# Optimization experiments

Hardware: AMD Instinct MI355X
Metric: run time of the kernel (lower is better)

Reference implementation:

```python
import jax, jax.numpy as jnp
import numpy as np

PS = 4          # patch size
C = 3           # channels
VOCAB = 512
D = 256         # embed dim
PD = PS * PS * C  # 48 patch dim


def _gelu(x):
    return jax.nn.gelu(x, approximate=False)  # torch nn.GELU default = exact erf


def setup_inputs() -> dict:
    key = jax.random.key(0)
    ks = jax.random.split(key, 16)
    frames = jax.random.uniform(ks[0], (32, 256, 256, 3), jnp.float32) * 255.0

    def lin(kw, kb, fan_in, fan_out):
        bound = 1.0 / np.sqrt(fan_in)
        w = jax.random.uniform(kw, (fan_out, fan_in), jnp.float32, -bound, bound)
        b = jax.random.uniform(kb, (fan_out,), jnp.float32, -bound, bound)
        return w, b

    enc_w1, enc_b1 = lin(ks[1], ks[2], PD, D)
    enc_w2, enc_b2 = lin(ks[3], ks[4], D, D)
    enc_w3, enc_b3 = lin(ks[5], ks[6], D, D)
    dec_w1, dec_b1 = lin(ks[7], ks[8], D, D)
    dec_w2, dec_b2 = lin(ks[9], ks[10], D, D)
    dec_w3, dec_b3 = lin(ks[11], ks[12], D, PD)
    codebook = jax.random.normal(ks[13], (VOCAB, D), jnp.float32) * 0.1
    return {
        'frames': frames,
        'enc_w1': enc_w1, 'enc_b1': enc_b1,
        'enc_w2': enc_w2, 'enc_b2': enc_b2,
        'enc_w3': enc_w3, 'enc_b3': enc_b3,
        'codebook': codebook,
        'dec_w1': dec_w1, 'dec_b1': dec_b1,
        'dec_w2': dec_w2, 'dec_b2': dec_b2,
        'dec_w3': dec_w3, 'dec_b3': dec_b3,
    }


def _patchify(x):  # [B,H,W,C] -> [B, N, ps*ps*C]
    B, H, W, Ch = x.shape
    h, w = H // PS, W // PS
    x = x.reshape(B, h, PS, w, PS, Ch).transpose(0, 1, 3, 2, 4, 5)
    return x.reshape(B, h * w, PS * PS * Ch)


def _unpatchify(p):  # [B, N, ps*ps*C] -> [B,H,W,C]
    B, N, _ = p.shape
    h = w = int(np.sqrt(N))
    p = p.reshape(B, h, w, PS, PS, C).transpose(0, 1, 3, 2, 4, 5)
    return p.reshape(B, h * PS, w * PS, C)


def reference(frames, enc_w1, enc_b1, enc_w2, enc_b2, enc_w3, enc_b3,
              codebook, dec_w1, dec_b1, dec_w2, dec_b2, dec_w3, dec_b3):
    x = frames / 255.0 * 2.0 - 1.0
    patches = _patchify(x)  # [B,N,48]
    # encoder MLP
    z = _gelu(patches @ enc_w1.T + enc_b1)
    z = _gelu(z @ enc_w2.T + enc_b2)
    z_e = z @ enc_w3.T + enc_b3  # [B,N,D]
    # nearest-codebook lookup (squared L2; argmin equals cdist argmin)
    d2 = (jnp.sum(z_e * z_e, -1, keepdims=True)
          - 2.0 * jnp.einsum('bnd,vd->bnv', z_e, codebook)
          + jnp.sum(codebook * codebook, -1))  # [B,N,V]
    tokens = jnp.argmin(d2, axis=-1)  # [B,N] int
    z_q = codebook[tokens]  # [B,N,D]
    z_q_st = z_e + jax.lax.stop_gradient(z_q - z_e)
    # decoder MLP
    y = _gelu(z_q_st @ dec_w1.T + dec_b1)
    y = _gelu(y @ dec_w2.T + dec_b2)
    y = y @ dec_w3.T + dec_b3  # [B,N,48]
    recon = _unpatchify(y)
    target = frames / 255.0 * 2.0 - 1.0
    recon_loss = jnp.mean((recon - target) ** 2)
    commitment_loss = jnp.mean((z_e - jax.lax.stop_gradient(z_q)) ** 2)
    codebook_loss = jnp.mean((z_q - jax.lax.stop_gradient(z_e)) ** 2)
    return recon, tokens, recon_loss, commitment_loss, codebook_loss
```

## Files before the change

### kernel.cpp

```cpp
#include <hip/hip_runtime.h>
#include <hip/hip_bf16.h>
#include <math.h>
#include <float.h>
#include <limits.h>

#define T_ROWS 131072

typedef __attribute__((ext_vector_type(8))) short short8;
typedef __attribute__((ext_vector_type(4))) float f32x4;

__device__ __forceinline__ float gelu_f(float x){
    return 0.5f * x * (1.0f + erff(x * 0.7071067811865475f));
}
__device__ __forceinline__ float bf2f(ushort u){
    union { unsigned int i; float f; } v; v.i = ((unsigned int)u) << 16; return v.f;
}
__device__ __forceinline__ ushort f2bf(float f){
    union { float f; unsigned int i; } v; v.f = f;
    unsigned int i = v.i;
    unsigned int r = (i + 0x7fffu + ((i >> 16) & 1u)) >> 16;
    return (ushort)r;
}
__device__ __forceinline__ void split3(float x, ushort &u0, ushort &u1, ushort &u2){
    union { float f; unsigned int i; } v; v.f = x;
    u0 = (ushort)(v.i >> 16);
    union { unsigned int i; float f; } h0; h0.i = ((unsigned int)u0) << 16;
    float r = x - h0.f;
    union { float f; unsigned int i; } vr; vr.f = r;
    u1 = (ushort)(vr.i >> 16);
    union { unsigned int i; float f; } h1; h1.i = ((unsigned int)u1) << 16;
    float r2 = r - h1.f;
    union { float f; unsigned int i; } v2; v2.f = r2;
    u2 = (ushort)(v2.i >> 16);
}

__global__ __launch_bounds__(256) void prep_kernel(
    const float* __restrict__ w2, const float* __restrict__ w3,
    const float* __restrict__ d1, const float* __restrict__ d2,
    const float* __restrict__ w1, const float* __restrict__ b1,
    const float* __restrict__ cb,
    ushort* __restrict__ w2s0, ushort* __restrict__ w2s1, ushort* __restrict__ w2s2,
    ushort* __restrict__ w3s0, ushort* __restrict__ w3s1, ushort* __restrict__ w3s2,
    ushort* __restrict__ w1b, ushort* __restrict__ w2b,
    float* __restrict__ cn, ushort* __restrict__ cbb,
    ushort* __restrict__ cbs0, ushort* __restrict__ cbs1, ushort* __restrict__ cbs2,
    ushort* __restrict__ w1p0, ushort* __restrict__ w1p1, ushort* __restrict__ w1p2,
    float* __restrict__ bias2)
{
    const int blk = blockIdx.x, tid = threadIdx.x;
    if (blk < 64){
        const int i = (blk*256 + tid)*4;
        float4 a = *(const float4*)(w2 + i);
        ushort4 s0, s1, s2;
        split3(a.x, s0.x, s1.x, s2.x); split3(a.y, s0.y, s1.y, s2.y);
        split3(a.z, s0.z, s1.z, s2.z); split3(a.w, s0.w, s1.w, s2.w);
        *(ushort4*)(w2s0+i)=s0; *(ushort4*)(w2s1+i)=s1; *(ushort4*)(w2s2+i)=s2;
        float4 b = *(const float4*)(w3 + i);
        split3(b.x, s0.x, s1.x, s2.x); split3(b.y, s0.y, s1.y, s2.y);
        split3(b.z, s0.z, s1.z, s2.z); split3(b.w, s0.w, s1.w, s2.w);
        *(ushort4*)(w3s0+i)=s0; *(ushort4*)(w3s1+i)=s1; *(ushort4*)(w3s2+i)=s2;
        float4 c = *(const float4*)(d1 + i);
        ushort4 u; u.x=f2bf(c.x); u.y=f2bf(c.y); u.z=f2bf(c.z); u.w=f2bf(c.w);
        *(ushort4*)(w1b+i) = u;
        float4 d = *(const float4*)(d2 + i);
        u.x=f2bf(d.x); u.y=f2bf(d.y); u.z=f2bf(d.z); u.w=f2bf(d.w);
        *(ushort4*)(w2b+i) = u;
    } else if (blk < 192){
        const int lane = tid & 63;
        const int code = (blk-64)*4 + (tid >> 6);
        float4 v = ((const float4*)(cb + (size_t)code*256))[lane];
        size_t off = (size_t)code*256 + lane*4;
        ushort4 u; u.x=f2bf(v.x); u.y=f2bf(v.y); u.z=f2bf(v.z); u.w=f2bf(v.w);
        *(ushort4*)(cbb + off) = u;
        ushort4 s0, s1, s2;
        split3(v.x, s0.x, s1.x, s2.x); split3(v.y, s0.y, s1.y, s2.y);
        split3(v.z, s0.z, s1.z, s2.z); split3(v.w, s0.w, s1.w, s2.w);
        *(ushort4*)(cbs0 + off) = s0;
        *(ushort4*)(cbs1 + off) = s1;
        *(ushort4*)(cbs2 + off) = s2;
        float s = v.x*v.x + v.y*v.y + v.z*v.z + v.w*v.w;
        #pragma unroll
        for (int m=1; m<64; m<<=1) s += __shfl_xor(s, m);
        if (lane == 0) cn[code] = s;
    } else if (blk < 208){
        const int idx = (blk-192)*256 + tid;
        const int n = idx >> 4, k = (idx & 15)*4;
        ushort4 s0 = {0,0,0,0}, s1 = {0,0,0,0}, s2 = {0,0,0,0};
        if (k < 48){
            float4 v = *(const float4*)(w1 + n*48 + k);
            split3(v.x, s0.x, s1.x, s2.x); split3(v.y, s0.y, s1.y, s2.y);
            split3(v.z, s0.z, s1.z, s2.z); split3(v.w, s0.w, s1.w, s2.w);
        }
        *(ushort4*)(w1p0 + n*64 + k) = s0;
        *(ushort4*)(w1p1 + n*64 + k) = s1;
        *(ushort4*)(w1p2 + n*64 + k) = s2;
    } else {
        float s = 0.0f;
        for (int k=0;k<48;++k) s += w1[tid*48 + k];
        bias2[tid] = b1[tid] - s;
    }
}

template<int KTOT, bool GELU, int LOADER, bool SCALE>
__global__ __launch_bounds__(256, 3) void split6_gemm(
    const float* __restrict__ Ain,
    const float* __restrict__ frames,
    const ushort* __restrict__ W0, const ushort* __restrict__ W1,
    const ushort* __restrict__ W2,
    const float* __restrict__ bias,
    float* __restrict__ Cout)
{
    __shared__ __align__(16) ushort Al[3][64][40];
    __shared__ __align__(16) ushort Wl[256][40];

    const int tid = threadIdx.x;
    const int m0 = blockIdx.x * 64;
    const int arow = tid >> 2, q = tid & 3;
    const int lane = tid & 63;
    const int w = tid >> 6;
    const int lr = lane & 15, lg = lane >> 4;

    const float* asrc = nullptr;
    int pbase = 0;
    if constexpr (LOADER == 0){
        asrc = Ain + (size_t)(m0 + arow)*KTOT + q*8;
    } else {
        int p = m0 + arow;
        int b = p >> 12, nl = p & 4095, hh = nl >> 6, ww = nl & 63;
        pbase = ((b*256 + hh*4)*256 + ww*4)*3;
    }
    const ushort* wsrc  = W0 + (size_t)tid*KTOT;
    const ushort* w1frag = W1 + (size_t)(w*64 + lr)*KTOT + lg*8;
    const ushort* w2frag = W2 + (size_t)(w*64 + lr)*KTOT + lg*8;

    f32x4 acc[4][4];
    #pragma unroll
    for (int mi=0;mi<4;++mi)
        #pragma unroll
        for (int ni=0;ni<4;++ni)
            acc[mi][ni] = (f32x4){0.f,0.f,0.f,0.f};

    for (int k0=0; k0<KTOT; k0+=32){
        float x[8];
        if constexpr (LOADER == 0){
            *(float4*)&x[0] = *(const float4*)(asrc + k0);
            *(float4*)&x[4] = *(const float4*)(asrc + k0 + 4);
        } else {
            #pragma unroll
            for (int j=0;j<2;++j){
                int kk = k0 + q*8 + j*4;
                float4 v = {0.f,0.f,0.f,0.f};
                if (kk < 48){
                    int ph = kk/12, rem = kk - ph*12;
                    v = *(const float4*)(frames + pbase + ph*768 + rem);
                }
                x[j*4+0]=v.x; x[j*4+1]=v.y; x[j*4+2]=v.z; x[j*4+3]=v.w;
            }
        }
        ushort t0[8], t1[8], t2[8];
        #pragma unroll
        for (int e=0;e<8;++e) split3(x[e], t0[e], t1[e], t2[e]);
        *(uint4*)&Al[0][arow][q*8] = *(const uint4*)t0;
        *(uint4*)&Al[1][arow][q*8] = *(const uint4*)t1;
        *(uint4*)&Al[2][arow][q*8] = *(const uint4*)t2;
        *(uint4*)&Wl[tid][0]  = *(const uint4*)(wsrc + k0);
        *(uint4*)&Wl[tid][8]  = *(const uint4*)(wsrc + k0 + 8);
        *(uint4*)&Wl[tid][16] = *(const uint4*)(wsrc + k0 + 16);
        *(uint4*)&Wl[tid][24] = *(const uint4*)(wsrc + k0 + 24);
        short8 b1v[4], b2v[4];
        #pragma unroll
        for (int ni=0;ni<4;++ni){
            b1v[ni] = *(const short8*)(w1frag + (size_t)ni*16*KTOT + k0);
            b2v[ni] = *(const short8*)(w2frag + (size_t)ni*16*KTOT + k0);
        }
        __syncthreads();

        short8 b0v[4];
        #pragma unroll
        for (int ni=0;ni<4;++ni)
            b0v[ni] = *(const short8*)&Wl[w*64 + ni*16 + lr][lg*8];
        #pragma unroll
        for (int mi=0;mi<4;++mi){
            short8 a0 = *(const short8*)&Al[0][mi*16 + lr][lg*8];
            short8 a1 = *(const short8*)&Al[1][mi*16 + lr][lg*8];
            short8 a2 = *(const short8*)&Al[2][mi*16 + lr][lg*8];
            #pragma unroll
            for (int ni=0;ni<4;++ni)
                acc[mi][ni] = __builtin_amdgcn_mfma_f32_16x16x32_bf16(a0, b0v[ni], acc[mi][ni], 0,0,0);
            #pragma unroll
            for (int ni=0;ni<4;++ni)
                acc[mi][ni] = __builtin_amdgcn_mfma_f32_16x16x32_bf16(a0, b1v[ni], acc[mi][ni], 0,0,0);
            #pragma unroll
            for (int ni=0;ni<4;++ni)
                acc[mi][ni] = __builtin_amdgcn_mfma_f32_16x16x32_bf16(a1, b0v[ni], acc[mi][ni], 0,0,0);
            #pragma unroll
            for (int ni=0;ni<4;++ni)
                acc[mi][ni] = __builtin_amdgcn_mfma_f32_16x16x32_bf16(a0, b2v[ni], acc[mi][ni], 0,0,0);
            #pragma unroll
            for (int ni=0;ni<4;++ni)
                acc[mi][ni] = __builtin_amdgcn_mfma_f32_16x16x32_bf16(a1, b1v[ni], acc[mi][ni], 0,0,0);
            #pragma unroll
            for (int ni=0;ni<4;++ni)
                acc[mi][ni] = __builtin_amdgcn_mfma_f32_16x16x32_bf16(a2, b0v[ni], acc[mi][ni], 0,0,0);
        }
        __syncthreads();
    }

    const float alpha = 2.0f/255.0f;
    float bn[4];
    #pragma unroll
    for (int ni=0;ni<4;++ni) bn[ni] = bias[w*64 + ni*16 + lr];
    #pragma unroll
    for (int mi=0;mi<4;++mi)
        #pragma unroll
        for (int ni=0;ni<4;++ni)
            #pragma unroll
            for (int r=0;r<4;++r){
                int row = m0 + mi*16 + lg*4 + r;
                float v;
                if (SCALE) v = fmaf(alpha, acc[mi][ni][r], bn[ni]);
                else       v = acc[mi][ni][r] + bn[ni];
                if (GELU) v = gelu_f(v);
                Cout[(size_t)row*256 + w*64 + ni*16 + lr] = v;
            }
}

#define INSERT1(dv, iv) do { \
    float _d = (dv); int _i = (iv); \
    if (_d < bd || (_d == bd && _i < bi)){ bd = _d; bi = _i; } \
} while(0)

__global__ __launch_bounds__(256, 3) void tokens_split6(
    const float* __restrict__ Zf,
    const ushort* __restrict__ C0, const ushort* __restrict__ C1,
    const ushort* __restrict__ C2,
    const float* __restrict__ cn,
    float2* __restrict__ partials,
    float* __restrict__ zz_out)
{
    __shared__ __align__(16) ushort Al[3][128][40];
    __shared__ __align__(16) ushort Wl[2][128][40];
    __shared__ float2 ptop[128][2];

    const int tid = threadIdx.x;
    const int m0 = blockIdx.x * 128;
    const int n0 = blockIdx.y * 128;
    const int srow = tid >> 1, shalf = (tid & 1) * 16;
    const int lane = tid & 63;
    const int w = tid >> 6;
    const int wm = (w >> 1) * 64, wn = (w & 1) * 64;
    const int lr = lane & 15, lg = lane >> 4;

    const float*  asrc = Zf + (size_t)(m0 + srow)*256 + shalf;
    const ushort* ws0  = C0 + (size_t)(n0 + srow)*256 + shalf;
    const ushort* ws1  = C1 + (size_t)(n0 + srow)*256 + shalf;
    const ushort* c2frag = C2 + (size_t)(n0 + wn + lr)*256 + lg*8;

    f32x4 acc[4][4];
    #pragma unroll
    for (int mi=0;mi<4;++mi)
        #pragma unroll
        for (int ni=0;ni<4;++ni)
            acc[mi][ni] = (f32x4){0.f,0.f,0.f,0.f};

    float zzp = 0.0f;

    for (int k0=0; k0<256; k0+=32){
        float x[16];
        *(float4*)&x[0]  = *(const float4*)(asrc + k0);
        *(float4*)&x[4]  = *(const float4*)(asrc + k0 + 4);
        *(float4*)&x[8]  = *(const float4*)(asrc + k0 + 8);
        *(float4*)&x[12] = *(const float4*)(asrc + k0 + 12);
        ushort t0[16], t1[16], t2[16];
        #pragma unroll
        for (int e=0;e<16;++e){
            split3(x[e], t0[e], t1[e], t2[e]);
            zzp = fmaf(x[e], x[e], zzp);
        }
        *(uint4*)&Al[0][srow][shalf]   = *(const uint4*)&t0[0];
        *(uint4*)&Al[0][srow][shalf+8] = *(const uint4*)&t0[8];
        *(uint4*)&Al[1][srow][shalf]   = *(const uint4*)&t1[0];
        *(uint4*)&Al[1][srow][shalf+8] = *(const uint4*)&t1[8];
        *(uint4*)&Al[2][srow][shalf]   = *(const uint4*)&t2[0];
        *(uint4*)&Al[2][srow][shalf+8] = *(const uint4*)&t2[8];
        *(uint4*)&Wl[0][srow][shalf]   = *(const uint4*)(ws0 + k0);
        *(uint4*)&Wl[0][srow][shalf+8] = *(const uint4*)(ws0 + k0 + 8);
        *(uint4*)&Wl[1][srow][shalf]   = *(const uint4*)(ws1 + k0);
        *(uint4*)&Wl[1][srow][shalf+8] = *(const uint4*)(ws1 + k0 + 8);
        short8 b2[4];
        #pragma unroll
        for (int ni=0;ni<4;++ni)
            b2[ni] = *(const short8*)(c2frag + (size_t)ni*16*256 + k0);
        __syncthreads();

        short8 b0[4], b1[4];
        #pragma unroll
        for (int ni=0;ni<4;++ni){
            b0[ni] = *(const short8*)&Wl[0][wn + ni*16 + lr][lg*8];
            b1[ni] = *(const short8*)&Wl[1][wn + ni*16 + lr][lg*8];
        }
        #pragma unroll
        for (int mi=0;mi<4;++mi){
            short8 a0 = *(const short8*)&Al[0][wm + mi*16 + lr][lg*8];
            short8 a1 = *(const short8*)&Al[1][wm + mi*16 + lr][lg*8];
            short8 a2 = *(const short8*)&Al[2][wm + mi*16 + lr][lg*8];
            #pragma unroll
            for (int ni=0;ni<4;++ni)
                acc[mi][ni] = __builtin_amdgcn_mfma_f32_16x16x32_bf16(a0, b0[ni], acc[mi][ni], 0,0,0);
            #pragma unroll
            for (int ni=0;ni<4;++ni)
                acc[mi][ni] = __builtin_amdgcn_mfma_f32_16x16x32_bf16(a0, b1[ni], acc[mi][ni], 0,0,0);
            #pragma unroll
            for (int ni=0;ni<4;++ni)
                acc[mi][ni] = __builtin_amdgcn_mfma_f32_16x16x32_bf16(a1, b0[ni], acc[mi][ni], 0,0,0);
            #pragma unroll
            for (int ni=0;ni<4;++ni)
                acc[mi][ni] = __builtin_amdgcn_mfma_f32_16x16x32_bf16(a0, b2[ni], acc[mi][ni], 0,0,0);
            #pragma unroll
            for (int ni=0;ni<4;++ni)
                acc[mi][ni] = __builtin_amdgcn_mfma_f32_16x16x32_bf16(a1, b1[ni], acc[mi][ni], 0,0,0);
            #pragma unroll
            for (int ni=0;ni<4;++ni)
                acc[mi][ni] = __builtin_amdgcn_mfma_f32_16x16x32_bf16(a2, b0[ni], acc[mi][ni], 0,0,0);
        }
        __syncthreads();
    }

    {
        float other = __shfl_xor(zzp, 1);
        if (blockIdx.y == 0 && (tid & 1) == 0)
            zz_out[m0 + srow] = zzp + other;
    }

    float cnl[4];
    #pragma unroll
    for (int ni=0;ni<4;++ni) cnl[ni] = cn[n0 + wn + ni*16 + lr];

    #pragma unroll
    for (int mi=0;mi<4;++mi)
        #pragma unroll
        for (int r=0;r<4;++r){
            float bd = FLT_MAX; int bi = INT_MAX;
            #pragma unroll
            for (int ni=0;ni<4;++ni){
                float d = cnl[ni] - 2.0f*acc[mi][ni][r];
                int col = n0 + wn + ni*16 + lr;
                INSERT1(d, col);
            }
            #pragma unroll
            for (int m=1; m<16; m<<=1){
                float od = __shfl_xor(bd, m);
                int   oi = __shfl_xor(bi, m);
                INSERT1(od, oi);
            }
            if (lr == 0)
                ptop[wm + mi*16 + lg*4 + r][w & 1] = make_float2(bd, (float)bi);
        }
    __syncthreads();
    if (tid < 128){
        float2 hA = ptop[tid][0], hB = ptop[tid][1];
        int   gA = (int)hA.y, gB = (int)hB.y;
        bool takeB = (hB.x < hA.x) || (hB.x == hA.x && gB < gA);
        partials[(size_t)(m0 + tid)*4 + blockIdx.y] = takeB ? hB : hA;
    }
}

__global__ __launch_bounds__(256) void token_reduce(
    const float* __restrict__ zz_out, const float2* __restrict__ partials,
    float* __restrict__ tokf, float* __restrict__ loss)
{
    const int tid = threadIdx.x;
    const int row = blockIdx.x*256 + tid;
    float2 p0 = partials[(size_t)row*4 + 0];
    float2 p1 = partials[(size_t)row*4 + 1];
    float2 p2 = partials[(size_t)row*4 + 2];
    float2 p3 = partials[(size_t)row*4 + 3];
    float d = p0.x; int g = (int)p0.y;
    if (p1.x < d || (p1.x == d && (int)p1.y < g)){ d = p1.x; g = (int)p1.y; }
    if (p2.x < d || (p2.x == d && (int)p2.y < g)){ d = p2.x; g = (int)p2.y; }
    if (p3.x < d || (p3.x == d && (int)p3.y < g)){ d = p3.x; g = (int)p3.y; }
    tokf[row] = (float)g;
    float cs = zz_out[row] + d;
    #pragma unroll
    for (int m=1; m<64; m<<=1) cs += __shfl_xor(cs, m);
    __shared__ float wsum[4];
    const int lane = tid & 63, w = tid >> 6;
    if (lane == 0) wsum[w] = cs;
    __syncthreads();
    if (tid == 0) atomicAdd(loss + 1, wsum[0]+wsum[1]+wsum[2]+wsum[3]);
}

template<int LOADER>
__global__ __launch_bounds__(256) void mfma_gemm(
    const ushort* __restrict__ Abf,
    const ushort* __restrict__ cbb,
    const float* __restrict__ tokf,
    const ushort* __restrict__ Wbf,
    const float* __restrict__ bias,
    ushort* __restrict__ Ybf)
{
    __shared__ __align__(16) ushort Al[128][40];
    __shared__ __align__(16) ushort Wl[128][40];

    const int tid = threadIdx.x;
    const int m0 = blockIdx.x * 128;
    const int n0 = blockIdx.y * 128;
    const int srow = tid >> 1, shalf = (tid & 1) * 16;
    const int lane = tid & 63;
    const int w = tid >> 6;
    const int wm = (w >> 1) * 64, wn = (w & 1) * 64;
    const int lr = lane & 15, lg = lane >> 4;

    const ushort* asrc;
    if constexpr (LOADER == 1){
        int g = (int)tokf[m0 + srow];
        asrc = cbb + (size_t)g*256 + shalf;
    } else {
        asrc = Abf + (size_t)(m0 + srow)*256 + shalf;
    }
    const ushort* wsrc = Wbf + (size_t)(n0 + srow)*256 + shalf;

    f32x4 acc[4][4];
    #pragma unroll
    for (int mi=0;mi<4;++mi)
        #pragma unroll
        for (int ni=0;ni<4;++ni)
            acc[mi][ni] = (f32x4){0.f,0.f,0.f,0.f};

    for (int k0=0; k0<256; k0+=32){
        *(uint4*)&Al[srow][shalf]   = *(const uint4*)(asrc + k0);
        *(uint4*)&Al[srow][shalf+8] = *(const uint4*)(asrc + k0 + 8);
        *(uint4*)&Wl[srow][shalf]   = *(const uint4*)(wsrc + k0);
        *(uint4*)&Wl[srow][shalf+8] = *(const uint4*)(wsrc + k0 + 8);
        __syncthreads();

        short8 af[4], bfr[4];
        #pragma unroll
        for (int mi=0;mi<4;++mi)
            af[mi] = *(const short8*)&Al[wm + mi*16 + lr][lg*8];
        #pragma unroll
        for (int ni=0;ni<4;++ni)
            bfr[ni] = *(const short8*)&Wl[wn + ni*16 + lr][lg*8];
        #pragma unroll
        for (int mi=0;mi<4;++mi)
            #pragma unroll
            for (int ni=0;ni<4;++ni)
                acc[mi][ni] = __builtin_amdgcn_mfma_f32_16x16x32_bf16(
                    af[mi], bfr[ni], acc[mi][ni], 0, 0, 0);
        __syncthreads();
    }

    float bn[4];
    #pragma unroll
    for (int ni=0;ni<4;++ni) bn[ni] = bias[n0 + wn + ni*16 + lr];
    #pragma unroll
    for (int mi=0;mi<4;++mi)
        #pragma unroll
        for (int ni=0;ni<4;++ni)
            #pragma unroll
            for (int r=0;r<4;++r){
                int row = m0 + wm + mi*16 + lg*4 + r;
                float v = acc[mi][ni][r] + bn[ni];
                v = gelu_f(v);
                Ybf[(size_t)row*256 + n0 + wn + ni*16 + lr] = f2bf(v);
            }
}

__global__ __launch_bounds__(256) void dec3_mfma(
    const ushort* __restrict__ Ain, const float* __restrict__ W,
    const float* __restrict__ bias, const float* __restrict__ frames,
    float* __restrict__ recon, float* __restrict__ loss)
{
    __shared__ __align__(16) ushort Al[256][40];
    __shared__ __align__(16) ushort Wl[48][40];

    const int tid = threadIdx.x;
    const int m0 = blockIdx.x * 256;
    const int lane = tid & 63;
    const int w = tid >> 6;
    const int lr = lane & 15, lg = lane >> 4;

    const ushort* asrc = Ain + (size_t)(m0 + tid)*256;

    f32x4 acc[4][3];
    #pragma unroll
    for (int mi=0;mi<4;++mi)
        #pragma unroll
        for (int ni=0;ni<3;++ni)
            acc[mi][ni] = (f32x4){0.f,0.f,0.f,0.f};

    for (int k0=0; k0<256; k0+=32){
        *(uint4*)&Al[tid][0]  = *(const uint4*)(asrc + k0);
        *(uint4*)&Al[tid][8]  = *(const uint4*)(asrc + k0 + 8);
        *(uint4*)&Al[tid][16] = *(const uint4*)(asrc + k0 + 16);
        *(uint4*)&Al[tid][24] = *(const uint4*)(asrc + k0 + 24);
        if (tid < 96){
            const int wrow = tid >> 1, wh = (tid & 1)*16;
            const float* wp = W + (size_t)wrow*256 + k0 + wh;
            float4 f0 = *(const float4*)(wp);
            float4 f1 = *(const float4*)(wp+4);
            float4 f2 = *(const float4*)(wp+8);
            float4 f3 = *(const float4*)(wp+12);
            ushort t[16];
            t[0]=f2bf(f0.x); t[1]=f2bf(f0.y); t[2]=f2bf(f0.z); t[3]=f2bf(f0.w);
            t[4]=f2bf(f1.x); t[5]=f2bf(f1.y); t[6]=f2bf(f1.z); t[7]=f2bf(f1.w);
            t[8]=f2bf(f2.x); t[9]=f2bf(f2.y); t[10]=f2bf(f2.z); t[11]=f2bf(f2.w);
            t[12]=f2bf(f3.x); t[13]=f2bf(f3.y); t[14]=f2bf(f3.z); t[15]=f2bf(f3.w);
            *(uint4*)&Wl[wrow][wh]   = *(const uint4*)&t[0];
            *(uint4*)&Wl[wrow][wh+8] = *(const uint4*)&t[8];
        }
        __syncthreads();

        short8 bfr[3];
        #pragma unroll
        for (int ni=0;ni<3;++ni)
            bfr[ni] = *(const short8*)&Wl[ni*16 + lr][lg*8];
        #pragma unroll
        for (int mi=0;mi<4;++mi){
            short8 af = *(const short8*)&Al[w*64 + mi*16 + lr][lg*8];
            #pragma unroll
            for (int ni=0;ni<3;++ni)
                acc[mi][ni] = __builtin_amdgcn_mfma_f32_16x16x32_bf16(
                    af, bfr[ni], acc[mi][ni], 0, 0, 0);
        }
        __syncthreads();
    }

    float bn[3]; int phv[3], remv[3];
    #pragma unroll
    for (int ni=0;ni<3;++ni){
        int col = ni*16 + lr;
        bn[ni] = bias[col];
        phv[ni] = col / 12;
        remv[ni] = col - phv[ni]*12;
    }
    const float sc = 2.0f/255.0f;
    float ls = 0.0f;
    #pragma unroll
    for (int mi=0;mi<4;++mi)
        #pragma unroll
        for (int ni=0;ni<3;++ni)
            #pragma unroll
            for (int r=0;r<4;++r){
                int p = m0 + w*64 + mi*16 + lg*4 + r;
                int b = p >> 12, nl = p & 4095, hh = nl >> 6, ww = nl & 63;
                size_t addr = (size_t)(((b*256 + hh*4 + phv[ni])*256 + ww*4)*3 + remv[ni]);
                float y = acc[mi][ni][r] + bn[ni];
                float t = frames[addr]*sc - 1.0f;
                float d = y - t;
                ls += d*d;
                recon[addr] = y;
            }

    #pragma unroll
    for (int off=32; off>0; off>>=1) ls += __shfl_down(ls, off);
    __shared__ float wsum[4];
    if (lane == 0) wsum[w] = ls;
    __syncthreads();
    if (tid == 0) atomicAdd(loss + 0, wsum[0]+wsum[1]+wsum[2]+wsum[3]);
}

__global__ void finalize_kernel(float* __restrict__ loss){
    if (threadIdx.x == 0 && blockIdx.x == 0){
        loss[0] = loss[0] * (1.0f/6291456.0f);
        float c = loss[1] * (1.0f/33554432.0f);
        loss[1] = c;
        loss[2] = c;
    }
}

extern "C" void kernel_launch(void* const* d_in, const int* in_sizes, int n_in,
                              void* d_out, int out_size, void* d_ws, size_t ws_size,
                              hipStream_t stream)
{
    (void)in_sizes; (void)n_in; (void)out_size; (void)ws_size;
    const float* frames   = (const float*)d_in[0];
    const float* enc_w1   = (const float*)d_in[1];
    const float* enc_b1   = (const float*)d_in[2];
    const float* enc_w2   = (const float*)d_in[3];
    const float* enc_b2   = (const float*)d_in[4];
    const float* enc_w3   = (const float*)d_in[5];
    const float* enc_b3   = (const float*)d_in[6];
    const float* codebook = (const float*)d_in[7];
    const float* dec_w1   = (const float*)d_in[8];
    const float* dec_b1   = (const float*)d_in[9];
    const float* dec_w2   = (const float*)d_in[10];
    const float* dec_b2   = (const float*)d_in[11];
    const float* dec_w3   = (const float*)d_in[12];
    const float* dec_b3   = (const float*)d_in[13];

    float* P = (float*)d_ws;
    float* Q = P + (size_t)33554432;
    float2* partials = (float2*)(Q + 18000000);
    ushort* Y1 = (ushort*)P;
    ushort* Y2 = (ushort*)Q;

    float* recon = (float*)d_out;
    float* tokf  = recon + 6291456;
    float* loss  = tokf + 131072;
    float*  cn   = recon;
    ushort* cbb  = (ushort*)(recon + 512);
    ushort* w1b  = (ushort*)(recon + 66048);
    ushort* w2b  = (ushort*)(recon + 98816);
    ushort* w2s0 = (ushort*)(recon + 131584);
    ushort* w2s1 = (ushort*)(recon + 164352);
    ushort* w2s2 = (ushort*)(recon + 197120);
    ushort* w3s0 = (ushort*)(recon + 229888);
    ushort* w3s1 = (ushort*)(recon + 262656);
    ushort* w3s2 = (ushort*)(recon + 295424);
    ushort* cbs0 = (ushort*)(recon + 328192);
    ushort* cbs1 = (ushort*)(recon + 393728);
    ushort* cbs2 = (ushort*)(recon + 459264);
    float*  zzb  = recon + 524800;
    ushort* w1p0 = (ushort*)(recon + 655872);
    ushort* w1p1 = (ushort*)(recon + 664064);
    ushort* w1p2 = (ushort*)(recon + 672256);
    float*  bias2 = recon + 680448;

    hipMemsetAsync(loss, 0, 3*sizeof(float), stream);

    dim3 blk(256);
    prep_kernel<<<dim3(209), blk, 0, stream>>>(enc_w2, enc_w3, dec_w1, dec_w2,
        enc_w1, enc_b1, codebook,
        w2s0, w2s1, w2s2, w3s0, w3s1, w3s2, w1b, w2b,
        cn, cbb, cbs0, cbs1, cbs2, w1p0, w1p1, w1p2, bias2);
    split6_gemm<64,  true, 1, true ><<<dim3(T_ROWS/64), blk, 0, stream>>>(nullptr, frames, w1p0, w1p1, w1p2, bias2, P);
    split6_gemm<256, true, 0, false><<<dim3(T_ROWS/64), blk, 0, stream>>>(P, nullptr, w2s0, w2s1, w2s2, enc_b2, Q);
    split6_gemm<256, false,0, false><<<dim3(T_ROWS/64), blk, 0, stream>>>(Q, nullptr, w3s0, w3s1, w3s2, enc_b3, P);
    tokens_split6<<<dim3(T_ROWS/128, 4), blk, 0, stream>>>(P, cbs0, cbs1, cbs2, cn, partials, zzb);
    token_reduce<<<dim3(T_ROWS/256), blk, 0, stream>>>(zzb, partials, tokf, loss);
    mfma_gemm<1><<<dim3(T_ROWS/128, 2), blk, 0, stream>>>(nullptr, cbb, tokf, w1b, dec_b1, Y1);
    mfma_gemm<0><<<dim3(T_ROWS/128, 2), blk, 0, stream>>>(Y1, nullptr, nullptr, w2b, dec_b2, Y2);
    dec3_mfma<<<dim3(T_ROWS/256), blk, 0, stream>>>(Y2, dec_w3, dec_b3, frames, recon, loss);
    finalize_kernel<<<dim3(1), dim3(64), 0, stream>>>(loss);
}
```

Baseline: 674.3 us.

## Precompute decoder outputs per codebook entry and gather by token

The decoder input is exactly a codebook row, so the decoder MLP is now run once over the 512 codebook entries to build a 512x48 output table. A new gather kernel then writes each patch's reconstruction by indexing that table with its token and accumulates the reconstruction loss with vectorized float4 accesses. This removes the three per-patch decoder GEMMs over 131072 rows. The table path matches the original only as long as z_q_st equals z_q in the forward pass, which the reference guarantees.

```diff
diff --git a/kernel.cpp b/kernel.cpp
--- a/kernel.cpp
+++ b/kernel.cpp
@@ -390,11 +390,8 @@
     if (tid == 0) atomicAdd(loss + 1, wsum[0]+wsum[1]+wsum[2]+wsum[3]);
 }
 
-template<int LOADER>
 __global__ __launch_bounds__(256) void mfma_gemm(
     const ushort* __restrict__ Abf,
-    const ushort* __restrict__ cbb,
-    const float* __restrict__ tokf,
     const ushort* __restrict__ Wbf,
     const float* __restrict__ bias,
     ushort* __restrict__ Ybf)
@@ -411,13 +408,7 @@
     const int wm = (w >> 1) * 64, wn = (w & 1) * 64;
     const int lr = lane & 15, lg = lane >> 4;
 
-    const ushort* asrc;
-    if constexpr (LOADER == 1){
-        int g = (int)tokf[m0 + srow];
-        asrc = cbb + (size_t)g*256 + shalf;
-    } else {
-        asrc = Abf + (size_t)(m0 + srow)*256 + shalf;
-    }
+    const ushort* asrc = Abf + (size_t)(m0 + srow)*256 + shalf;
     const ushort* wsrc = Wbf + (size_t)(n0 + srow)*256 + shalf;
 
     f32x4 acc[4][4];
@@ -466,10 +457,9 @@
             }
 }
 
-__global__ __launch_bounds__(256) void dec3_mfma(
+__global__ __launch_bounds__(256) void dec3_table(
     const ushort* __restrict__ Ain, const float* __restrict__ W,
-    const float* __restrict__ bias, const float* __restrict__ frames,
-    float* __restrict__ recon, float* __restrict__ loss)
+    const float* __restrict__ bias, float* __restrict__ Rt)
 {
     __shared__ __align__(16) ushort Al[256][40];
     __shared__ __align__(16) ushort Wl[48][40];
@@ -526,35 +516,47 @@
         __syncthreads();
     }
 
-    float bn[3]; int phv[3], remv[3];
     #pragma unroll
     for (int ni=0;ni<3;++ni){
-        int col = ni*16 + lr;
-        bn[ni] = bias[col];
-        phv[ni] = col / 12;
-        remv[ni] = col - phv[ni]*12;
-    }
+        const int col = ni*16 + lr;
+        const float bn = bias[col];
+        #pragma unroll
+        for (int mi=0;mi<4;++mi)
+            #pragma unroll
+            for (int r=0;r<4;++r){
+                int row = m0 + w*64 + mi*16 + lg*4 + r;
+                Rt[row*48 + col] = acc[mi][ni][r] + bn;
+            }
+    }
+}
+
+__global__ __launch_bounds__(256) void gather_recon(
+    const float* __restrict__ Rt, const float* __restrict__ tokf,
+    const float* __restrict__ frames, float* __restrict__ recon,
+    float* __restrict__ loss)
+{
+    const int tid = threadIdx.x;
+    const int idx = blockIdx.x*256 + tid;
+    const int p = idx >> 2, ph = idx & 3;
+    const int g = (int)tokf[p];
+    int b = p >> 12, nl = p & 4095, hh = nl >> 6, ww = nl & 63;
+    size_t base = (size_t)(((b*256 + hh*4 + ph)*256 + ww*4)*3);
+    const float* rp = Rt + g*48 + ph*12;
     const float sc = 2.0f/255.0f;
     float ls = 0.0f;
     #pragma unroll
-    for (int mi=0;mi<4;++mi)
-        #pragma unroll
-        for (int ni=0;ni<3;++ni)
-            #pragma unroll
-            for (int r=0;r<4;++r){
-                int p = m0 + w*64 + mi*16 + lg*4 + r;
-                int b = p >> 12, nl = p & 4095, hh = nl >> 6, ww = nl & 63;
-                size_t addr = (size_t)(((b*256 + hh*4 + phv[ni])*256 + ww*4)*3 + remv[ni]);
-                float y = acc[mi][ni][r] + bn[ni];
-                float t = frames[addr]*sc - 1.0f;
-                float d = y - t;
-                ls += d*d;
-                recon[addr] = y;
-            }
-
+    for (int j=0;j<3;++j){
+        float4 y = *(const float4*)(rp + j*4);
+        float4 f = *(const float4*)(frames + base + j*4);
+        float t0=f.x*sc-1.0f, t1=f.y*sc-1.0f, t2=f.z*sc-1.0f, t3=f.w*sc-1.0f;
+        float d0=y.x-t0, d1=y.y-t1, d2=y.z-t2, d3=y.w-t3;
+        ls += d0*d0 + d1*d1 + d2*d2 + d3*d3;
+        *(float4*)(recon + base + j*4) = y;
+    }
     #pragma unroll
     for (int off=32; off>0; off>>=1) ls += __shfl_down(ls, off);
     __shared__ float wsum[4];
+    int lane = tid & 63, w = tid >> 6;
     if (lane == 0) wsum[w] = ls;
     __syncthreads();
     if (tid == 0) atomicAdd(loss + 0, wsum[0]+wsum[1]+wsum[2]+wsum[3]);
@@ -592,8 +594,9 @@
     float* P = (float*)d_ws;
     float* Q = P + (size_t)33554432;
     float2* partials = (float2*)(Q + 18000000);
-    ushort* Y1 = (ushort*)P;
-    ushort* Y2 = (ushort*)Q;
+    ushort* L1 = (ushort*)P;
+    ushort* L2 = (ushort*)(P + 65536);
+    float*  Rt = P + 131072;
 
     float* recon = (float*)d_out;
     float* tokf  = recon + 6291456;
@@ -629,8 +632,9 @@
     split6_gemm<256, false,0, false><<<dim3(T_ROWS/64), blk, 0, stream>>>(Q, nullptr, w3s0, w3s1, w3s2, enc_b3, P);
     tokens_split6<<<dim3(T_ROWS/128, 4), blk, 0, stream>>>(P, cbs0, cbs1, cbs2, cn, partials, zzb);
     token_reduce<<<dim3(T_ROWS/256), blk, 0, stream>>>(zzb, partials, tokf, loss);
-    mfma_gemm<1><<<dim3(T_ROWS/128, 2), blk, 0, stream>>>(nullptr, cbb, tokf, w1b, dec_b1, Y1);
-    mfma_gemm<0><<<dim3(T_ROWS/128, 2), blk, 0, stream>>>(Y1, nullptr, nullptr, w2b, dec_b2, Y2);
-    dec3_mfma<<<dim3(T_ROWS/256), blk, 0, stream>>>(Y2, dec_w3, dec_b3, frames, recon, loss);
+    mfma_gemm<<<dim3(4, 2), blk, 0, stream>>>(cbb, w1b, dec_b1, L1);
+    mfma_gemm<<<dim3(4, 2), blk, 0, stream>>>(L1, w2b, dec_b2, L2);
+    dec3_table<<<dim3(2), blk, 0, stream>>>(L2, dec_w3, dec_b3, Rt);
+    gather_recon<<<dim3(T_ROWS*4/256), blk, 0, stream>>>(Rt, tokf, frames, recon, loss);
     finalize_kernel<<<dim3(1), dim3(64), 0, stream>>>(loss);
 }
```

New measurement: 597.7 us. 11.4% less time.
